# Kernel optimization log

Hardware: AMD Instinct MI355X
Metric: run time of the kernel (lower is better)

## Reference

```python
import jax, jax.numpy as jnp
import numpy as np
from jax import lax

N = 100_000      # active voxels
C = 64           # nIn == nOut
K = 343          # 7*7*7 depthwise taps
HID = 4 * C      # pointwise expansion
EPS = 1e-5
CENTER = K // 2  # self offset


def setup_inputs() -> dict:
    key = jax.random.key(0)
    ks = jax.random.split(key, 10)
    x_feat = jax.random.normal(ks[0], (N, C), dtype=jnp.float32)
    nbr = jax.random.randint(ks[1], (N, K), 0, N, dtype=jnp.int32)
    valid = jax.random.uniform(ks[2], (N, K)) < 0.25
    nbr = jnp.where(valid, nbr, jnp.int32(N))
    nbr = nbr.at[:, CENTER].set(jnp.arange(N, dtype=jnp.int32))  # submanifold: center is self
    W1 = jax.random.normal(ks[3], (K, C), dtype=jnp.float32) * 0.05
    b1 = jax.random.normal(ks[4], (C,), dtype=jnp.float32) * 0.02
    gamma = jnp.ones((C,), dtype=jnp.float32)
    beta = jnp.zeros((C,), dtype=jnp.float32)
    W2 = jax.random.normal(ks[5], (C, HID), dtype=jnp.float32) * (1.0 / np.sqrt(C))
    b2 = jax.random.normal(ks[6], (HID,), dtype=jnp.float32) * 0.02
    W3 = jax.random.normal(ks[7], (HID, C), dtype=jnp.float32) * (1.0 / np.sqrt(HID))
    b3 = jax.random.normal(ks[8], (C,), dtype=jnp.float32) * 0.02
    return {"x_feat": x_feat, "nbr_idx": nbr, "W1": W1, "b1": b1,
            "gamma": gamma, "beta": beta, "W2": W2, "b2": b2, "W3": W3, "b3": b3}


def _depthwise_submanifold(feat, nbr_idx, W1, b1):
    # feat [N,C]; nbr_idx [N,K] with sentinel N -> zero contribution
    feat_pad = jnp.concatenate([feat, jnp.zeros((1, feat.shape[1]), feat.dtype)], axis=0)
    def step(acc, xs):
        idx_k, w_k = xs                       # [N], [C]
        return acc + feat_pad[idx_k] * w_k, None  # gather + per-channel MAC
    acc0 = jnp.zeros_like(feat)
    out, _ = lax.scan(step, acc0, (nbr_idx.T, W1))  # scan over K=343 taps
    return out + b1


def _groupnorm1(h, gamma, beta):
    # num_groups=1 over channels, per active site
    mu = jnp.mean(h, axis=-1, keepdims=True)
    var = jnp.var(h, axis=-1, keepdims=True)
    return (h - mu) * lax.rsqrt(var + EPS) * gamma + beta


def reference(x_feat, nbr_idx, W1, b1, gamma, beta, W2, b2, W3, b3):
    h = _depthwise_submanifold(x_feat, nbr_idx, W1, b1)  # conv1 (depthwise 7^3)
    h = _groupnorm1(h, gamma, beta)                      # norm
    h = h @ W2 + b2                                      # conv2 (1x1x1, C->4C)
    h = jax.nn.gelu(h, approximate=False)                # exact GELU (torch default)
    h = h @ W3 + b3                                      # conv3 (1x1x1, 4C->C)
    return h + x_feat                                    # residual add
```

## Files before the change

kernel.cpp:

```cpp
#include <hip/hip_runtime.h>
#include <hip/hip_fp16.h>
#include <math.h>

#define CH    64
#define KT    343
#define HIDD  256

typedef __attribute__((ext_vector_type(8))) _Float16 half8;
typedef __attribute__((ext_vector_type(4))) _Float16 half4;
typedef __attribute__((ext_vector_type(4))) float f32x4;
struct H24 { __half2 x, y, z, w; };

#define MEMBAR() asm volatile("" ::: "memory")

__global__ __launch_bounds__(256) void prep_w_kernel(
    const float* __restrict__ W1, const float* __restrict__ W2,
    const float* __restrict__ W3, _Float16* __restrict__ W1h,
    _Float16* __restrict__ W2Th, _Float16* __restrict__ W3Th) {
  const int t = blockIdx.x * 256 + threadIdx.x;
  const int step = gridDim.x * 256;
  for (int e = t; e < KT * CH; e += step) W1h[e] = (_Float16)W1[e];
  for (int e = t; e < CH * HIDD; e += step) {
    int k = e >> 8, n = e & 255;
    W2Th[n * CH + k] = (_Float16)W2[e];
  }
  for (int e = t; e < HIDD * CH; e += step) {
    int k = e >> 6, n = e & 63;
    W3Th[n * HIDD + k] = (_Float16)W3[e];
  }
}

__global__ __launch_bounds__(256) void xcast_kernel(
    const float* __restrict__ x, _Float16* __restrict__ xh, int nelem) {
  const int tot4 = nelem / 4 + 16;
  for (int q = blockIdx.x * 256 + threadIdx.x; q < tot4; q += gridDim.x * 256) {
    const int eb = q * 4;
    float4 v = (eb < nelem) ? *(const float4*)(x + eb) : make_float4(0.f, 0.f, 0.f, 0.f);
    half4 o;
    o[0] = (_Float16)v.x; o[1] = (_Float16)v.y;
    o[2] = (_Float16)v.z; o[3] = (_Float16)v.w;
    *(half4*)(xh + eb) = o;
  }
}

#define ISSUE8(buf, vi)                                                     \
  { _Pragma("unroll") for (int p = 0; p < 8; ++p) {                         \
      const int idx_ = __builtin_amdgcn_ds_bpermute(pb + 4 * p, (vi));      \
      buf[p] = *(const uint4*)(xb + (((unsigned)idx_ << 7) + (unsigned)e16)); } }

#define CONSUME8(buf, tapbase)                                              \
  { _Pragma("unroll") for (int p = 0; p < 8; ++p) {                         \
      const uint4 wq_ = *(const uint4*)&W1s[(((tapbase) + p) << 7) + e16];  \
      const H24 gh_ = __builtin_bit_cast(H24, buf[p]);                      \
      const H24 wh_ = __builtin_bit_cast(H24, wq_);                         \
      acc0 = __hfma2(gh_.x, wh_.x, acc0);                                   \
      acc1 = __hfma2(gh_.y, wh_.y, acc1);                                   \
      acc2 = __hfma2(gh_.z, wh_.z, acc2);                                   \
      acc3 = __hfma2(gh_.w, wh_.w, acc3); } }

__global__ __launch_bounds__(256, 3) void fused_kernel(
    const _Float16* __restrict__ xh, const float* __restrict__ x,
    const int* __restrict__ nbr, const _Float16* __restrict__ W1h,
    const float* __restrict__ b1, const float* __restrict__ gamma,
    const float* __restrict__ beta, const _Float16* __restrict__ W2Th,
    const float* __restrict__ b2, const _Float16* __restrict__ W3Th,
    const float* __restrict__ b3, float* __restrict__ out, int N) {
  __shared__ __align__(16) char W1s[43904];
  __shared__ __align__(16) _Float16 hs[32][CH + 8];
  _Float16 (*gs)[HIDD + 8] = (_Float16 (*)[HIDD + 8])W1s;

  const int t = threadIdx.x;
  const int wvid = t >> 6;
  const int lane = t & 63;
  const int g = lane >> 3;
  const int e = lane & 7;
  const int e16 = e << 4;
  const int pb = (lane & 56) << 2;
  const int vbase = blockIdx.x * 32;
  const int vb = __builtin_amdgcn_readfirstlane(vbase + wvid * 8);

  {
    const uint4* src = (const uint4*)W1h;
    uint4* dst = (uint4*)W1s;
    for (int q = t; q < 2744; q += 256) dst[q] = src[q];
  }

  const int* nbw = nbr + (size_t)vb * KT;
  const int nbo = g * KT + e;
  const char* xb = (const char*)xh;

  __half2 acc0 = __float2half2_rn(0.f), acc1 = acc0, acc2 = acc0, acc3 = acc0;

  uint4 ga[8], gb[8];
  int viA = nbw[nbo];
  int viB = nbw[nbo + 8];
  ISSUE8(ga, viA);
  __syncthreads();

  for (int ck = 0; ck < 42; ck += 2) {
    const int viC = nbw[nbo + ((ck + 2 < 42) ? (ck + 2) * 8 : 335)];
    MEMBAR();
    ISSUE8(gb, viB);
    MEMBAR();
    CONSUME8(ga, ck * 8);
    const int viD = nbw[nbo + ((ck + 3 < 42) ? (ck + 3) * 8 : 335)];
    MEMBAR();
    if (ck + 2 < 42) ISSUE8(ga, viC);
    MEMBAR();
    CONSUME8(gb, ck * 8 + 8);
    viB = viD;
  }

  {
    uint4 gt[7];
#pragma unroll
    for (int p = 0; p < 7; ++p) {
      const int idx = __builtin_amdgcn_ds_bpermute(pb + 4 * (p + 1), viB);
      gt[p] = *(const uint4*)(xb + (((unsigned)idx << 7) + (unsigned)e16));
    }
    MEMBAR();
#pragma unroll
    for (int p = 0; p < 7; ++p) {
      const uint4 wq = *(const uint4*)&W1s[((336 + p) << 7) + e16];
      const H24 gh = __builtin_bit_cast(H24, gt[p]);
      const H24 wh = __builtin_bit_cast(H24, wq);
      acc0 = __hfma2(gh.x, wh.x, acc0);
      acc1 = __hfma2(gh.y, wh.y, acc1);
      acc2 = __hfma2(gh.z, wh.z, acc2);
      acc3 = __hfma2(gh.w, wh.w, acc3);
    }
  }

  float fa[8];
  fa[0] = __low2float(acc0); fa[1] = __high2float(acc0);
  fa[2] = __low2float(acc1); fa[3] = __high2float(acc1);
  fa[4] = __low2float(acc2); fa[5] = __high2float(acc2);
  fa[6] = __low2float(acc3); fa[7] = __high2float(acc3);
  {
    float4 blo = *(const float4*)(b1 + e * 8);
    float4 bhi = *(const float4*)(b1 + e * 8 + 4);
    fa[0] += blo.x; fa[1] += blo.y; fa[2] += blo.z; fa[3] += blo.w;
    fa[4] += bhi.x; fa[5] += bhi.y; fa[6] += bhi.z; fa[7] += bhi.w;
  }
  float s = 0.f, ss = 0.f;
#pragma unroll
  for (int d = 0; d < 8; ++d) { s += fa[d]; ss += fa[d] * fa[d]; }
  s += __shfl_xor(s, 1); ss += __shfl_xor(ss, 1);
  s += __shfl_xor(s, 2); ss += __shfl_xor(ss, 2);
  s += __shfl_xor(s, 4); ss += __shfl_xor(ss, 4);
  const float mu = s * (1.0f / 64.0f);
  const float var = ss * (1.0f / 64.0f) - mu * mu;
  const float inv = rsqrtf(var + 1e-5f);
  {
    float4 glo = *(const float4*)(gamma + e * 8);
    float4 ghi = *(const float4*)(gamma + e * 8 + 4);
    float4 tlo = *(const float4*)(beta + e * 8);
    float4 thi = *(const float4*)(beta + e * 8 + 4);
    const float gm[8] = {glo.x, glo.y, glo.z, glo.w, ghi.x, ghi.y, ghi.z, ghi.w};
    const float bt[8] = {tlo.x, tlo.y, tlo.z, tlo.w, thi.x, thi.y, thi.z, thi.w};
    half8 hv;
#pragma unroll
    for (int d = 0; d < 8; ++d)
      hv[d] = (_Float16)((fa[d] - mu) * inv * gm[d] + bt[d]);
    *(half8*)&hs[wvid * 8 + g][e * 8] = hv;
  }
  __syncthreads();

  const int row16 = lane & 15, quad = lane >> 4;
  half8 afr[2][2];
#pragma unroll
  for (int rt = 0; rt < 2; ++rt)
#pragma unroll
    for (int ks = 0; ks < 2; ++ks)
      afr[rt][ks] = *(const half8*)&hs[rt * 16 + row16][ks * 32 + quad * 8];

#pragma unroll
  for (int cl = 0; cl < 4; ++cl) {
    const int n = wvid * 64 + cl * 16 + row16;
    f32x4 a0 = {0.f, 0.f, 0.f, 0.f}, a1 = {0.f, 0.f, 0.f, 0.f};
#pragma unroll
    for (int ks = 0; ks < 2; ++ks) {
      half8 bfr = *(const half8*)(W2Th + (size_t)n * CH + ks * 32 + quad * 8);
      a0 = __builtin_amdgcn_mfma_f32_16x16x32_f16(afr[0][ks], bfr, a0, 0, 0, 0);
      a1 = __builtin_amdgcn_mfma_f32_16x16x32_f16(afr[1][ks], bfr, a1, 0, 0, 0);
    }
    const float bias = b2[n];
#pragma unroll
    for (int r = 0; r < 4; ++r) {
      float z0 = a0[r] + bias;
      float z1 = a1[r] + bias;
      gs[quad * 4 + r][n]      = (_Float16)(0.5f * z0 * (1.0f + erff(z0 * 0.70710678118654752f)));
      gs[16 + quad * 4 + r][n] = (_Float16)(0.5f * z1 * (1.0f + erff(z1 * 0.70710678118654752f)));
    }
  }
  __syncthreads();

  f32x4 o0 = {0.f, 0.f, 0.f, 0.f}, o1 = {0.f, 0.f, 0.f, 0.f};
  const int oc = wvid * 16 + row16;
#pragma unroll
  for (int ks = 0; ks < 8; ++ks) {
    half8 bfr = *(const half8*)(W3Th + (size_t)oc * HIDD + ks * 32 + quad * 8);
    half8 a20 = *(const half8*)&gs[row16][ks * 32 + quad * 8];
    half8 a21 = *(const half8*)&gs[16 + row16][ks * 32 + quad * 8];
    o0 = __builtin_amdgcn_mfma_f32_16x16x32_f16(a20, bfr, o0, 0, 0, 0);
    o1 = __builtin_amdgcn_mfma_f32_16x16x32_f16(a21, bfr, o1, 0, 0, 0);
  }
  const float bias3 = b3[oc];
#pragma unroll
  for (int r = 0; r < 4; ++r) {
    size_t v0 = (size_t)vbase + quad * 4 + r;
    size_t v1 = (size_t)vbase + 16 + quad * 4 + r;
    out[v0 * CH + oc] = o0[r] + bias3 + x[v0 * CH + oc];
    out[v1 * CH + oc] = o1[r] + bias3 + x[v1 * CH + oc];
  }
}

extern "C" void kernel_launch(void* const* d_in, const int* in_sizes, int n_in,
                              void* d_out, int out_size, void* d_ws, size_t ws_size,
                              hipStream_t stream) {
  const float* x_feat = (const float*)d_in[0];
  const int*   nbr    = (const int*)d_in[1];
  const float* W1     = (const float*)d_in[2];
  const float* b1     = (const float*)d_in[3];
  const float* gamma  = (const float*)d_in[4];
  const float* beta   = (const float*)d_in[5];
  const float* W2     = (const float*)d_in[6];
  const float* b2     = (const float*)d_in[7];
  const float* W3     = (const float*)d_in[8];
  const float* b3     = (const float*)d_in[9];
  float* out = (float*)d_out;

  const int N = in_sizes[0] / CH;

  char* ws = (char*)d_ws;
  size_t off = 0;
  _Float16* xh = (_Float16*)(ws + off);
  off += (((size_t)(N + 1) * CH * 2) + 255) & ~(size_t)255;
  _Float16* W1h = (_Float16*)(ws + off);
  off += ((size_t)KT * CH * 2 + 255) & ~(size_t)255;
  _Float16* W2Th = (_Float16*)(ws + off);
  off += ((size_t)HIDD * CH * 2 + 255) & ~(size_t)255;
  _Float16* W3Th = (_Float16*)(ws + off);

  hipLaunchKernelGGL(prep_w_kernel, dim3(32), dim3(256), 0, stream,
                     W1, W2, W3, W1h, W2Th, W3Th);
  hipLaunchKernelGGL(xcast_kernel, dim3(1024), dim3(256), 0, stream,
                     x_feat, xh, N * CH);
  hipLaunchKernelGGL(fused_kernel, dim3(N / 32), dim3(256), 0, stream,
                     xh, x_feat, nbr, W1h, b1, gamma, beta,
                     W2Th, b2, W3Th, b3, out, N);
}
```

Baseline: 440.7 us.

## Compact neighbor table to valid taps before fused depthwise gather

Adds a pre-pass that scans the neighbor table, drops sentinel entries and writes a compacted per-group list. Each entry packs the voxel index and tap id together. The fused kernel then gathers and accumulates only the valid neighbors, looking up the weight by the stored tap id. This is meant to cut the roughly 75% of gathers and FMAs spent on empty taps. In exchange it reads the neighbor table twice, writes and re-reads a large workspace table, and adds an atomic allocation step. It falls back to the old kernel when the workspace is too small.

```diff
diff --git a/kernel.cpp b/kernel.cpp
--- a/kernel.cpp
+++ b/kernel.cpp
@@ -43,6 +43,215 @@
   }
 }
 
+__global__ __launch_bounds__(256) void compact_kernel(
+    const int* __restrict__ nbr, int* __restrict__ table,
+    int* __restrict__ hdrBase, int* __restrict__ hdrLen,
+    int* __restrict__ counter, int capEntries, int N) {
+  const int wvid = threadIdx.x >> 6;
+  const int lane = threadIdx.x & 63;
+  const int gr = blockIdx.x * 4 + wvid;
+  const int g = lane >> 3, e = lane & 7;
+  const int* np = nbr + (size_t)(gr * 8 + g) * KT;
+
+  int cnt = 0;
+  for (int j = 0; j < 43; ++j) {
+    const int k = j * 8 + e;
+    const int ld = (k < KT) ? np[k] : N;
+    const unsigned long long m = __ballot(ld < N);
+    cnt += __popcll(m & (0xFFull << (8 * g)));
+  }
+  int mx = cnt;
+  mx = max(mx, __shfl_xor(mx, 8));
+  mx = max(mx, __shfl_xor(mx, 16));
+  mx = max(mx, __shfl_xor(mx, 32));
+  const int nch8 = (mx + 7) & ~7;
+  int b0 = 0;
+  if (lane == 0) b0 = atomicAdd(counter, nch8 * 8);
+  const int base = __shfl(b0, 0);
+
+  if (base + nch8 * 8 <= capEntries) {
+    if (lane == 0) { hdrBase[gr] = base; hdrLen[gr] = nch8; }
+    int cnt2 = 0;
+    for (int j = 0; j < 43; ++j) {
+      const int k = j * 8 + e;
+      const int ld = (k < KT) ? np[k] : N;
+      const bool valid = ld < N;
+      const unsigned long long m = __ballot(valid);
+      const unsigned byte = (unsigned)((m >> (8 * g)) & 0xFFull);
+      if (valid) {
+        const int pos = cnt2 + __popc(byte & ((1u << e) - 1u));
+        table[base + pos * 8 + g] = ld | (k << 17);
+      }
+      cnt2 += __popc(byte);
+    }
+    for (int p = cnt2 + e; p < nch8; p += 8)
+      table[base + p * 8 + g] = N | (342 << 17);
+  } else if (lane == 0) {
+    hdrBase[gr] = 0; hdrLen[gr] = 0;
+  }
+}
+
+#define ISSUE8C(buf, ent, vi)                                               \
+  { _Pragma("unroll") for (int p = 0; p < 8; ++p) {                         \
+      ent[p] = __builtin_amdgcn_ds_bpermute(pb + 4 * p, (vi));              \
+      const unsigned idx_ = (unsigned)ent[p] & 0x1FFFFu;                    \
+      buf[p] = *(const uint4*)(xb + ((idx_ << 7) + (unsigned)e16)); } }
+
+#define CONSUME8C(buf, ent)                                                 \
+  { _Pragma("unroll") for (int p = 0; p < 8; ++p) {                         \
+      const unsigned tap_ = (unsigned)ent[p] >> 17;                         \
+      const uint4 wq_ = *(const uint4*)&W1s[(tap_ << 7) + e16];             \
+      const H24 gh_ = __builtin_bit_cast(H24, buf[p]);                      \
+      const H24 wh_ = __builtin_bit_cast(H24, wq_);                         \
+      acc0 = __hfma2(gh_.x, wh_.x, acc0);                                   \
+      acc1 = __hfma2(gh_.y, wh_.y, acc1);                                   \
+      acc2 = __hfma2(gh_.z, wh_.z, acc2);                                   \
+      acc3 = __hfma2(gh_.w, wh_.w, acc3); } }
+
+__global__ __launch_bounds__(256, 3) void fused_compact_kernel(
+    const _Float16* __restrict__ xh, const float* __restrict__ x,
+    const int* __restrict__ table, const int* __restrict__ hdrBase,
+    const int* __restrict__ hdrLen, const _Float16* __restrict__ W1h,
+    const float* __restrict__ b1, const float* __restrict__ gamma,
+    const float* __restrict__ beta, const _Float16* __restrict__ W2Th,
+    const float* __restrict__ b2, const _Float16* __restrict__ W3Th,
+    const float* __restrict__ b3, float* __restrict__ out, int N) {
+  __shared__ __align__(16) char W1s[43904];
+  __shared__ __align__(16) _Float16 hs[32][CH + 8];
+  _Float16 (*gs)[HIDD + 8] = (_Float16 (*)[HIDD + 8])W1s;
+
+  const int t = threadIdx.x;
+  const int wvid = t >> 6;
+  const int lane = t & 63;
+  const int g = lane >> 3;
+  const int e = lane & 7;
+  const int e16 = e << 4;
+  const int pb = (lane & 56) << 2;
+  const int vbase = blockIdx.x * 32;
+
+  {
+    const uint4* src = (const uint4*)W1h;
+    uint4* dst = (uint4*)W1s;
+    for (int q = t; q < 2744; q += 256) dst[q] = src[q];
+  }
+
+  const int grp = __builtin_amdgcn_readfirstlane(blockIdx.x * 4 + wvid);
+  const int base = hdrBase[grp];
+  const int nch = hdrLen[grp] >> 3;
+  const int* tb = table + base;
+  const int o = e * 8 + g;
+  const char* xb = (const char*)xh;
+
+  __half2 acc0 = __float2half2_rn(0.f), acc1 = acc0, acc2 = acc0, acc3 = acc0;
+  uint4 ga[8], gb[8];
+  int ea[8], eb[8];
+
+  int vi = tb[o];
+  ISSUE8C(ga, ea, vi);
+  __syncthreads();
+
+  int c = 1;
+  for (; c + 1 < nch; c += 2) {
+    const int viB = tb[c * 64 + o];
+    MEMBAR(); ISSUE8C(gb, eb, viB); MEMBAR();
+    CONSUME8C(ga, ea);
+    const int viA = tb[(c + 1) * 64 + o];
+    MEMBAR(); ISSUE8C(ga, ea, viA); MEMBAR();
+    CONSUME8C(gb, eb);
+  }
+  if (c < nch) {
+    const int viB = tb[c * 64 + o];
+    MEMBAR(); ISSUE8C(gb, eb, viB); MEMBAR();
+    CONSUME8C(ga, ea);
+    CONSUME8C(gb, eb);
+  } else {
+    CONSUME8C(ga, ea);
+  }
+
+  float fa[8];
+  fa[0] = __low2float(acc0); fa[1] = __high2float(acc0);
+  fa[2] = __low2float(acc1); fa[3] = __high2float(acc1);
+  fa[4] = __low2float(acc2); fa[5] = __high2float(acc2);
+  fa[6] = __low2float(acc3); fa[7] = __high2float(acc3);
+  {
+    float4 blo = *(const float4*)(b1 + e * 8);
+    float4 bhi = *(const float4*)(b1 + e * 8 + 4);
+    fa[0] += blo.x; fa[1] += blo.y; fa[2] += blo.z; fa[3] += blo.w;
+    fa[4] += bhi.x; fa[5] += bhi.y; fa[6] += bhi.z; fa[7] += bhi.w;
+  }
+  float s = 0.f, ss = 0.f;
+#pragma unroll
+  for (int d = 0; d < 8; ++d) { s += fa[d]; ss += fa[d] * fa[d]; }
+  s += __shfl_xor(s, 1); ss += __shfl_xor(ss, 1);
+  s += __shfl_xor(s, 2); ss += __shfl_xor(ss, 2);
+  s += __shfl_xor(s, 4); ss += __shfl_xor(ss, 4);
+  const float mu = s * (1.0f / 64.0f);
+  const float var = ss * (1.0f / 64.0f) - mu * mu;
+  const float inv = rsqrtf(var + 1e-5f);
+  {
+    float4 glo = *(const float4*)(gamma + e * 8);
+    float4 ghi = *(const float4*)(gamma + e * 8 + 4);
+    float4 tlo = *(const float4*)(beta + e * 8);
+    float4 thi = *(const float4*)(beta + e * 8 + 4);
+    const float gm[8] = {glo.x, glo.y, glo.z, glo.w, ghi.x, ghi.y, ghi.z, ghi.w};
+    const float bt[8] = {tlo.x, tlo.y, tlo.z, tlo.w, thi.x, thi.y, thi.z, thi.w};
+    half8 hv;
+#pragma unroll
+    for (int d = 0; d < 8; ++d)
+      hv[d] = (_Float16)((fa[d] - mu) * inv * gm[d] + bt[d]);
+    *(half8*)&hs[wvid * 8 + g][e * 8] = hv;
+  }
+  __syncthreads();
+
+  const int row16 = lane & 15, quad = lane >> 4;
+  half8 afr[2][2];
+#pragma unroll
+  for (int rt = 0; rt < 2; ++rt)
+#pragma unroll
+    for (int ks = 0; ks < 2; ++ks)
+      afr[rt][ks] = *(const half8*)&hs[rt * 16 + row16][ks * 32 + quad * 8];
+
+#pragma unroll
+  for (int cl = 0; cl < 4; ++cl) {
+    const int n = wvid * 64 + cl * 16 + row16;
+    f32x4 a0 = {0.f, 0.f, 0.f, 0.f}, a1 = {0.f, 0.f, 0.f, 0.f};
+#pragma unroll
+    for (int ks = 0; ks < 2; ++ks) {
+      half8 bfr = *(const half8*)(W2Th + (size_t)n * CH + ks * 32 + quad * 8);
+      a0 = __builtin_amdgcn_mfma_f32_16x16x32_f16(afr[0][ks], bfr, a0, 0, 0, 0);
+      a1 = __builtin_amdgcn_mfma_f32_16x16x32_f16(afr[1][ks], bfr, a1, 0, 0, 0);
+    }
+    const float bias = b2[n];
+#pragma unroll
+    for (int r = 0; r < 4; ++r) {
+      float z0 = a0[r] + bias;
+      float z1 = a1[r] + bias;
+      gs[quad * 4 + r][n]      = (_Float16)(0.5f * z0 * (1.0f + erff(z0 * 0.70710678118654752f)));
+      gs[16 + quad * 4 + r][n] = (_Float16)(0.5f * z1 * (1.0f + erff(z1 * 0.70710678118654752f)));
+    }
+  }
+  __syncthreads();
+
+  f32x4 o0 = {0.f, 0.f, 0.f, 0.f}, o1 = {0.f, 0.f, 0.f, 0.f};
+  const int oc = wvid * 16 + row16;
+#pragma unroll
+  for (int ks = 0; ks < 8; ++ks) {
+    half8 bfr = *(const half8*)(W3Th + (size_t)oc * HIDD + ks * 32 + quad * 8);
+    half8 a20 = *(const half8*)&gs[row16][ks * 32 + quad * 8];
+    half8 a21 = *(const half8*)&gs[16 + row16][ks * 32 + quad * 8];
+    o0 = __builtin_amdgcn_mfma_f32_16x16x32_f16(a20, bfr, o0, 0, 0, 0);
+    o1 = __builtin_amdgcn_mfma_f32_16x16x32_f16(a21, bfr, o1, 0, 0, 0);
+  }
+  const float bias3 = b3[oc];
+#pragma unroll
+  for (int r = 0; r < 4; ++r) {
+    size_t v0 = (size_t)vbase + quad * 4 + r;
+    size_t v1 = (size_t)vbase + 16 + quad * 4 + r;
+    out[v0 * CH + oc] = o0[r] + bias3 + x[v0 * CH + oc];
+    out[v1 * CH + oc] = o1[r] + bias3 + x[v1 * CH + oc];
+  }
+}
+
 #define ISSUE8(buf, vi)                                                     \
   { _Pragma("unroll") for (int p = 0; p < 8; ++p) {                         \
       const int idx_ = __builtin_amdgcn_ds_bpermute(pb + 4 * p, (vi));      \
@@ -90,7 +299,6 @@
   const char* xb = (const char*)xh;
 
   __half2 acc0 = __float2half2_rn(0.f), acc1 = acc0, acc2 = acc0, acc3 = acc0;
-
   uint4 ga[8], gb[8];
   int viA = nbw[nbo];
   int viB = nbw[nbo + 8];
@@ -99,9 +307,7 @@
 
   for (int ck = 0; ck < 42; ck += 2) {
     const int viC = nbw[nbo + ((ck + 2 < 42) ? (ck + 2) * 8 : 335)];
-    MEMBAR();
-    ISSUE8(gb, viB);
-    MEMBAR();
+    MEMBAR(); ISSUE8(gb, viB); MEMBAR();
     CONSUME8(ga, ck * 8);
     const int viD = nbw[nbo + ((ck + 3 < 42) ? (ck + 3) * 8 : 335)];
     MEMBAR();
@@ -110,7 +316,6 @@
     CONSUME8(gb, ck * 8 + 8);
     viB = viD;
   }
-
   {
     uint4 gt[7];
 #pragma unroll
@@ -231,22 +436,37 @@
   float* out = (float*)d_out;
 
   const int N = in_sizes[0] / CH;
+  const int GN = N / 8;
 
   char* ws = (char*)d_ws;
   size_t off = 0;
-  _Float16* xh = (_Float16*)(ws + off);
-  off += (((size_t)(N + 1) * CH * 2) + 255) & ~(size_t)255;
-  _Float16* W1h = (_Float16*)(ws + off);
-  off += ((size_t)KT * CH * 2 + 255) & ~(size_t)255;
-  _Float16* W2Th = (_Float16*)(ws + off);
-  off += ((size_t)HIDD * CH * 2 + 255) & ~(size_t)255;
-  _Float16* W3Th = (_Float16*)(ws + off);
+  auto al = [](size_t v) { return (v + 255) & ~(size_t)255; };
+  _Float16* xh = (_Float16*)(ws + off);   off += al((size_t)(N + 1) * CH * 2);
+  _Float16* W1h = (_Float16*)(ws + off);  off += al((size_t)KT * CH * 2);
+  _Float16* W2Th = (_Float16*)(ws + off); off += al((size_t)HIDD * CH * 2);
+  _Float16* W3Th = (_Float16*)(ws + off); off += al((size_t)CH * HIDD * 2);
+  int* hdrBase = (int*)(ws + off);        off += al((size_t)GN * 4);
+  int* hdrLen = (int*)(ws + off);         off += al((size_t)GN * 4);
+  int* counter = (int*)(ws + off);        off += 256;
+  int* table = (int*)(ws + off);
+  const long long capEntries = 12000000;
+  const size_t need = off + (size_t)capEntries * 4;
 
   hipLaunchKernelGGL(prep_w_kernel, dim3(32), dim3(256), 0, stream,
                      W1, W2, W3, W1h, W2Th, W3Th);
   hipLaunchKernelGGL(xcast_kernel, dim3(1024), dim3(256), 0, stream,
                      x_feat, xh, N * CH);
-  hipLaunchKernelGGL(fused_kernel, dim3(N / 32), dim3(256), 0, stream,
-                     xh, x_feat, nbr, W1h, b1, gamma, beta,
-                     W2Th, b2, W3Th, b3, out, N);
-}
+
+  if (ws_size >= need) {
+    hipMemsetAsync(counter, 0, sizeof(int), stream);
+    hipLaunchKernelGGL(compact_kernel, dim3(GN / 4), dim3(256), 0, stream,
+                       nbr, table, hdrBase, hdrLen, counter, (int)capEntries, N);
+    hipLaunchKernelGGL(fused_compact_kernel, dim3(N / 32), dim3(256), 0, stream,
+                       xh, x_feat, table, hdrBase, hdrLen, W1h, b1, gamma, beta,
+                       W2Th, b2, W3Th, b3, out, N);
+  } else {
+    hipLaunchKernelGGL(fused_kernel, dim3(N / 32), dim3(256), 0, stream,
+                       xh, x_feat, nbr, W1h, b1, gamma, beta,
+                       W2Th, b2, W3Th, b3, out, N);
+  }
+}
```

Measured after the change: 585.3 us. 32.8% more time.
